# Kernel optimization log

Measured on AMD Instinct MI355X. Metric: run time of the kernel, lower is better.

Reference implementation:

```python
import jax, jax.numpy as jnp
import numpy as np

N_NODES = 50000
N_EDGES = 600000
D = 128
REL_DIM = 100
N_REL = 40
NEG_SLOPE = 0.2


def setup_inputs() -> dict:
    key = jax.random.key(0)
    ks = jax.random.split(key, 9)
    return {
        "node_features": jax.random.normal(ks[0], (N_NODES, D), jnp.float32),
        "edge_index": jax.random.randint(ks[1], (2, N_EDGES), 0, N_NODES, jnp.int64 if jax.config.jax_enable_x64 else jnp.int32),
        "edge_type": jax.random.randint(ks[2], (N_EDGES,), 0, N_REL, jnp.int32),
        "W": jax.random.normal(ks[3], (D, D), jnp.float32) * (1.0 / np.sqrt(D)),
        "W_r": jax.random.normal(ks[4], (REL_DIM, D), jnp.float32) * (1.0 / np.sqrt(REL_DIM)),
        "a": jax.random.normal(ks[5], (3 * D,), jnp.float32) * (1.0 / np.sqrt(3 * D)),
        "W_res": jax.random.normal(ks[6], (D, D), jnp.float32) * (1.0 / np.sqrt(D)),
        "b_res": jax.random.normal(ks[7], (D,), jnp.float32) * 0.01,
        "rel_emb": jax.random.normal(ks[8], (N_REL, REL_DIM), jnp.float32),
    }


def _segment_softmax(logits, seg_ids, num_segments):
    # numerically stable softmax over edges grouped by destination node
    seg_max = jax.ops.segment_max(logits, seg_ids, num_segments=num_segments)
    seg_max = jnp.where(jnp.isfinite(seg_max), seg_max, 0.0)
    e = jnp.exp(logits - seg_max[seg_ids])
    seg_sum = jax.ops.segment_sum(e, seg_ids, num_segments=num_segments)
    return e / (seg_sum[seg_ids] + 1e-16)


def reference(node_features, edge_index, edge_type, W, W_r, a, W_res, b_res, rel_emb):
    src = edge_index[0]  # x_j (source / message sender)
    dst = edge_index[1]  # x_i (target / aggregation index)

    h = node_features @ W                      # [N, D]
    h_rel = rel_emb[edge_type] @ W_r           # [E, D]
    h_src = h[src]                             # [E, D]
    h_dst = h[dst]                             # [E, D]

    # attention logit per edge: a . cat(W x_i, W x_j, W_r r_e), LeakyReLU(0.2)
    logit = h_dst @ a[:D] + h_src @ a[D:2 * D] + h_rel @ a[2 * D:]  # [E]
    logit = jax.nn.leaky_relu(logit, NEG_SLOPE)

    alpha = _segment_softmax(logit, dst, N_NODES)  # [E]

    agg = jax.ops.segment_sum(h_src * alpha[:, None], dst, num_segments=N_NODES)  # [N, D]

    out = agg + node_features @ W_res + b_res  # residual connection
    # LayerG: SELU then dropout (identity in eval mode)
    return jax.nn.selu(out)
```

## Files before the change

kernel.cpp:

```cpp
#include <hip/hip_runtime.h>
#include <hip/hip_bf16.h>

typedef __attribute__((ext_vector_type(8))) short bf16x8;
typedef __attribute__((ext_vector_type(4))) float f32x4;

#define LDS_STRIDE 528
#define CAP 64

__device__ __forceinline__ unsigned short f2bf(float f) {
    union { float f; unsigned int u; } v; v.f = f;
    unsigned int r = (v.u + 0x7FFF + ((v.u >> 16) & 1)) >> 16;
    return (unsigned short)r;
}
__device__ __forceinline__ float bf2f(unsigned int hbits) {
    union { unsigned int u; float f; } v; v.u = hbits << 16;
    return v.f;
}

__global__ __launch_bounds__(256) void setup_kernel(
    int* __restrict__ counts, int N,
    const float* __restrict__ W, const float* __restrict__ W_res,
    unsigned short* __restrict__ WbPack,
    const float* __restrict__ W_r, const float* __restrict__ a,
    const float* __restrict__ rel_emb, float* __restrict__ rl,
    int n_rel, int rel_dim, int zb)
{
    __shared__ float a3[128];
    __shared__ float wa[128];
    int bid = blockIdx.x;
    int tid = threadIdx.x;
    if (bid < zb) {
        int i = bid * 256 + tid;
        if (i < N) counts[i] = 0;
        return;
    }
    if (bid < zb + 16) {
        int g = (bid - zb) * 256 + tid;
        int t = g >> 8;
        int s = (g >> 6) & 3;
        int lane = g & 63;
        int ncol = ((t & 7) << 4) + (lane & 15);
        int k0 = s * 32 + ((lane >> 4) << 3);
        const float* srcw = (t < 8) ? W : W_res;
        unsigned short* dst = WbPack + ((size_t)(t * 4 + s) * 64 + lane) * 8;
        #pragma unroll
        for (int j = 0; j < 8; ++j) dst[j] = f2bf(srcw[(size_t)(k0 + j) * 128 + ncol]);
        return;
    }
    if (tid < 128) {
        a3[tid] = a[256 + tid];
    }
    __syncthreads();
    if (tid < rel_dim) {
        float s = 0.f;
        for (int d = 0; d < 128; ++d) s += W_r[tid * 128 + d] * a3[d];
        wa[tid] = s;
    }
    __syncthreads();
    if (tid < n_rel) {
        float s = 0.f;
        for (int k = 0; k < rel_dim; ++k) s += rel_emb[tid * rel_dim + k] * wa[k];
        rl[tid] = s;
    }
}

__global__ __launch_bounds__(256) void gemm_edge_kernel(
    const float* __restrict__ X, const unsigned short* __restrict__ WbPack,
    const float* __restrict__ b_res, const float* __restrict__ a,
    unsigned short* __restrict__ hb, unsigned short* __restrict__ resb,
    float* __restrict__ p, float* __restrict__ q, int M,
    const int* __restrict__ src, const int* __restrict__ dst_i, const int* __restrict__ etype,
    int* __restrict__ counts, unsigned int* __restrict__ slots, int E, int EB)
{
    __shared__ __align__(16) unsigned char smem[64 * LDS_STRIDE];
    __shared__ float pq_s[128];
    const int tid = threadIdx.x;
    const int bid = blockIdx.x;

    const bool is_edge = (bid < 2 * EB) && (bid & 1);
    if (is_edge) {
        const int base = (bid >> 1) * 2048 + tid;
        #pragma unroll
        for (int k = 0; k < 8; ++k) {
            int e = base + k * 256;
            if (e < E) {
                int d = __builtin_nontemporal_load(dst_i + e);
                int s = __builtin_nontemporal_load(src + e);
                int t = __builtin_nontemporal_load(etype + e);
                int rk = atomicAdd(&counts[d], 1);
                if (rk < CAP)
                    slots[(size_t)d * CAP + rk] = (unsigned int)s | ((unsigned int)t << 16);
            }
        }
        return;
    }
    const int gid = (bid < 2 * EB) ? (bid >> 1) : (bid - EB);

    const int lane = tid & 63;
    const int wave = tid >> 6;
    const int rowbase = gid * 64;
    const int c16 = lane & 15;
    const int kq = lane >> 4;

    if (tid < 128) pq_s[tid] = 0.f;

    bf16x8 wfrag[4][4];
    #pragma unroll
    for (int tt = 0; tt < 4; ++tt)
        #pragma unroll
        for (int s = 0; s < 4; ++s)
            wfrag[tt][s] = *(const bf16x8*)(WbPack + ((size_t)((wave * 4 + tt) * 4 + s) * 64 + lane) * 8);

    float bres[4];
    #pragma unroll
    for (int tt = 0; tt < 4; ++tt) {
        int t = wave * 4 + tt;
        bres[tt] = (t >= 8) ? b_res[(t - 8) * 16 + c16] : 0.f;
    }
    float pa[4], qa[4];
    #pragma unroll
    for (int tt = 0; tt < 4; ++tt) {
        int col = (wave * 4 + tt) * 16 + c16;
        pa[tt] = (wave < 2) ? a[col] : 0.f;
        qa[tt] = (wave < 2) ? a[128 + col] : 0.f;
    }

    #pragma unroll
    for (int j = 0; j < 8; ++j) {
        int ch = j * 256 + tid;
        int r = ch >> 5;
        int c = ch & 31;
        int gr = rowbase + r; if (gr >= M) gr = M - 1;
        float4 v = *(const float4*)(X + (size_t)gr * 128 + c * 4);
        unsigned int u0 = ((unsigned)f2bf(v.y) << 16) | f2bf(v.x);
        unsigned int u1 = ((unsigned)f2bf(v.w) << 16) | f2bf(v.z);
        *(uint2*)(smem + r * LDS_STRIDE + c * 8) = make_uint2(u0, u1);
    }
    __syncthreads();

    f32x4 acc[4][4];
    #pragma unroll
    for (int rt = 0; rt < 4; ++rt)
        #pragma unroll
        for (int tt = 0; tt < 4; ++tt) acc[rt][tt] = (f32x4){0.f, 0.f, 0.f, 0.f};

    #pragma unroll
    for (int s = 0; s < 4; ++s) {
        #pragma unroll
        for (int rt = 0; rt < 4; ++rt) {
            int row = rt * 16 + c16;
            bf16x8 af = *(const bf16x8*)(smem + row * LDS_STRIDE + s * 64 + kq * 16);
            #pragma unroll
            for (int tt = 0; tt < 4; ++tt)
                acc[rt][tt] = __builtin_amdgcn_mfma_f32_16x16x32_bf16(af, wfrag[tt][s], acc[rt][tt], 0, 0, 0);
        }
    }
    __syncthreads();

    if (wave < 2) {
        #pragma unroll
        for (int rt = 0; rt < 4; ++rt) {
            #pragma unroll
            for (int i = 0; i < 4; ++i) {
                float pp = 0.f, qq = 0.f;
                #pragma unroll
                for (int tt = 0; tt < 4; ++tt) {
                    pp += acc[rt][tt][i] * pa[tt];
                    qq += acc[rt][tt][i] * qa[tt];
                }
                #pragma unroll
                for (int d = 1; d < 16; d <<= 1) {
                    pp += __shfl_xor(pp, d, 64);
                    qq += __shfl_xor(qq, d, 64);
                }
                if (c16 == 0) {
                    int r = rt * 16 + kq * 4 + i;
                    atomicAdd(&pq_s[r], pp);
                    atomicAdd(&pq_s[64 + r], qq);
                }
            }
        }
    }

    #pragma unroll
    for (int rt = 0; rt < 4; ++rt) {
        #pragma unroll
        for (int tt = 0; tt < 4; ++tt) {
            int colall = (wave * 4 + tt) * 16 + c16;
            #pragma unroll
            for (int i = 0; i < 4; ++i) {
                int row = rt * 16 + kq * 4 + i;
                *(unsigned short*)(smem + row * LDS_STRIDE + colall * 2) = f2bf(acc[rt][tt][i] + bres[tt]);
            }
        }
    }
    __syncthreads();

    #pragma unroll
    for (int j = 0; j < 4; ++j) {
        int ch = j * 256 + tid;
        int r = ch >> 4;
        int c = ch & 15;
        int gr = rowbase + r;
        uint4 hv = *(const uint4*)(smem + r * LDS_STRIDE + c * 16);
        uint4 rv = *(const uint4*)(smem + r * LDS_STRIDE + 256 + c * 16);
        if (gr < M) {
            *(uint4*)(hb + (size_t)gr * 128 + c * 8) = hv;
            *(uint4*)(resb + (size_t)gr * 128 + c * 8) = rv;
        }
    }
    if (tid < 64) {
        int gr = rowbase + tid;
        if (gr < M) { p[gr] = pq_s[tid]; q[gr] = pq_s[64 + tid]; }
    }
}

__global__ __launch_bounds__(256) void agg_kernel(
    const unsigned short* __restrict__ hb, const unsigned short* __restrict__ resb,
    const float* __restrict__ p, const float* __restrict__ q, const float* __restrict__ rl,
    const int* __restrict__ counts, const unsigned int* __restrict__ slots,
    float* __restrict__ out, int N, int n_rel)
{
    __shared__ float rls[64];
    if (threadIdx.x < n_rel) rls[threadIdx.x] = rl[threadIdx.x];
    __syncthreads();

    const int tid = threadIdx.x;
    const int lane = tid & 63;
    const int sub = lane & 31;
    const int shbase = lane & 32;
    int node = blockIdx.x * 8 + ((tid >> 6) << 1) + (lane >> 5);
    if (node >= N) return;
    int nn = min(counts[node], CAP);

    float pnode = p[node];
    float a0 = 0.f, a1 = 0.f, a2 = 0.f, a3 = 0.f;
    float ssum = 0.f;
    const unsigned short* hsub = hb + sub * 4;

    for (int c = 0; c < nn; c += 32) {
        int m = min(32, nn - c);
        float se = 0.f;
        int sv = 0;
        if (sub < m) {
            unsigned int pk = slots[(size_t)node * CAP + c + sub];
            sv = (int)(pk & 0xffffu);
            int t = (int)(pk >> 16);
            float l = pnode + q[sv] + rls[t];
            l = (l > 0.f) ? l : 0.2f * l;
            se = __expf(l);
        }
        ssum += se;

        int j = 0;
        for (; j + 7 < m; j += 8) {
            float w[8]; int r[8]; uint2 v[8];
            #pragma unroll
            for (int u = 0; u < 8; ++u) { w[u] = __shfl(se, shbase + j + u); r[u] = __shfl(sv, shbase + j + u); }
            #pragma unroll
            for (int u = 0; u < 8; ++u) v[u] = *(const uint2*)(hsub + (size_t)r[u] * 128);
            #pragma unroll
            for (int u = 0; u < 8; ++u) {
                a0 += w[u] * bf2f(v[u].x & 0xffff);
                a1 += w[u] * bf2f(v[u].x >> 16);
                a2 += w[u] * bf2f(v[u].y & 0xffff);
                a3 += w[u] * bf2f(v[u].y >> 16);
            }
        }
        for (; j + 3 < m; j += 4) {
            float w[4]; int r[4]; uint2 v[4];
            #pragma unroll
            for (int u = 0; u < 4; ++u) { w[u] = __shfl(se, shbase + j + u); r[u] = __shfl(sv, shbase + j + u); }
            #pragma unroll
            for (int u = 0; u < 4; ++u) v[u] = *(const uint2*)(hsub + (size_t)r[u] * 128);
            #pragma unroll
            for (int u = 0; u < 4; ++u) {
                a0 += w[u] * bf2f(v[u].x & 0xffff);
                a1 += w[u] * bf2f(v[u].x >> 16);
                a2 += w[u] * bf2f(v[u].y & 0xffff);
                a3 += w[u] * bf2f(v[u].y >> 16);
            }
        }
        for (; j < m; ++j) {
            float w = __shfl(se, shbase + j);
            int r = __shfl(sv, shbase + j);
            uint2 v = *(const uint2*)(hsub + (size_t)r * 128);
            a0 += w * bf2f(v.x & 0xffff);
            a1 += w * bf2f(v.x >> 16);
            a2 += w * bf2f(v.y & 0xffff);
            a3 += w * bf2f(v.y >> 16);
        }
    }

    #pragma unroll
    for (int d = 1; d < 32; d <<= 1) ssum += __shfl_xor(ssum, d, 64);
    float inv = 1.0f / (ssum + 1e-16f);
    a0 *= inv; a1 *= inv; a2 *= inv; a3 *= inv;

    uint2 rv = *(const uint2*)(resb + (size_t)node * 128 + sub * 4);
    float o0 = a0 + bf2f(rv.x & 0xffff), o1 = a1 + bf2f(rv.x >> 16);
    float o2 = a2 + bf2f(rv.y & 0xffff), o3 = a3 + bf2f(rv.y >> 16);
    const float SC = 1.0507009873554805f, AL = 1.6732632423543772f;
    o0 = (o0 > 0.f) ? SC * o0 : SC * AL * (__expf(o0) - 1.f);
    o1 = (o1 > 0.f) ? SC * o1 : SC * AL * (__expf(o1) - 1.f);
    o2 = (o2 > 0.f) ? SC * o2 : SC * AL * (__expf(o2) - 1.f);
    o3 = (o3 > 0.f) ? SC * o3 : SC * AL * (__expf(o3) - 1.f);
    f32x4 ov = (f32x4){o0, o1, o2, o3};
    __builtin_nontemporal_store(ov, (f32x4*)(out + (size_t)node * 128 + sub * 4));
}

extern "C" void kernel_launch(void* const* d_in, const int* in_sizes, int n_in,
                              void* d_out, int out_size, void* d_ws, size_t ws_size,
                              hipStream_t stream)
{
    const float* X      = (const float*)d_in[0];
    const int*   ei     = (const int*)d_in[1];
    const int*   etype  = (const int*)d_in[2];
    const float* W      = (const float*)d_in[3];
    const float* W_r    = (const float*)d_in[4];
    const float* a      = (const float*)d_in[5];
    const float* W_res  = (const float*)d_in[6];
    const float* b_res  = (const float*)d_in[7];
    const float* rel_emb= (const float*)d_in[8];

    const int N = in_sizes[0] / 128;
    const int E = in_sizes[2];
    const int n_rel = in_sizes[8] / 100;
    const int* src = ei;
    const int* dst = ei + E;

    char* w = (char*)d_ws;
    auto alloc = [&](size_t bytes) -> void* {
        void* ptr = (void*)w;
        w += (bytes + 255) & ~(size_t)255;
        return ptr;
    };
    unsigned short* WbPack = (unsigned short*)alloc((size_t)16 * 4 * 64 * 8 * 2);
    unsigned short* hb     = (unsigned short*)alloc((size_t)N * 128 * 2);
    unsigned short* resb   = (unsigned short*)alloc((size_t)N * 128 * 2);
    float* p       = (float*)alloc((size_t)N * 4);
    float* q       = (float*)alloc((size_t)N * 4);
    float* rl      = (float*)alloc(64 * 4);
    int*   counts  = (int*)alloc((size_t)N * 4);
    unsigned int* slots = (unsigned int*)alloc((size_t)N * CAP * 4);
    float* out     = (float*)d_out;

    const int zb = (N + 255) / 256;
    const int gemm_blocks = (N + 63) / 64;
    const int agg_blocks = (N + 7) / 8;
    const int edge_blocks = (E + 2047) / 2048;
    const int fused_blocks = gemm_blocks + edge_blocks;

    setup_kernel<<<zb + 17, 256, 0, stream>>>(counts, N, W, W_res, WbPack,
                                              W_r, a, rel_emb, rl, n_rel, 100, zb);
    gemm_edge_kernel<<<fused_blocks, 256, 0, stream>>>(X, WbPack, b_res, a, hb, resb, p, q, N,
                                                       src, dst, etype, counts, slots, E, edge_blocks);
    agg_kernel<<<agg_blocks, 256, 0, stream>>>(hb, resb, p, q, rl, counts, slots, out, N, n_rel);
}
```

Baseline: 173.6 us.

## Fold edge bucketing into every GEMM block instead of separate edge blocks

Drops the interleaved edge-only blocks and gives each GEMM block a share of edges (up to 1024). The edge indices are loaded at kernel start into registers and scattered with atomics after the GEMM epilogue, so the load latency hides behind the matmul. This cuts the block count and the idle edge blocks, but adds register pressure (12 ints per thread). It also assumes EPB stays at or below 1024, which holds here (E/gemm_blocks rounds up to 768).

```diff
diff --git a/kernel.cpp b/kernel.cpp
--- a/kernel.cpp
+++ b/kernel.cpp
@@ -70,31 +70,24 @@
     unsigned short* __restrict__ hb, unsigned short* __restrict__ resb,
     float* __restrict__ p, float* __restrict__ q, int M,
     const int* __restrict__ src, const int* __restrict__ dst_i, const int* __restrict__ etype,
-    int* __restrict__ counts, unsigned int* __restrict__ slots, int E, int EB)
+    int* __restrict__ counts, unsigned int* __restrict__ slots, int E, int EPB)
 {
     __shared__ __align__(16) unsigned char smem[64 * LDS_STRIDE];
     __shared__ float pq_s[128];
     const int tid = threadIdx.x;
-    const int bid = blockIdx.x;
-
-    const bool is_edge = (bid < 2 * EB) && (bid & 1);
-    if (is_edge) {
-        const int base = (bid >> 1) * 2048 + tid;
-        #pragma unroll
-        for (int k = 0; k < 8; ++k) {
-            int e = base + k * 256;
-            if (e < E) {
-                int d = __builtin_nontemporal_load(dst_i + e);
-                int s = __builtin_nontemporal_load(src + e);
-                int t = __builtin_nontemporal_load(etype + e);
-                int rk = atomicAdd(&counts[d], 1);
-                if (rk < CAP)
-                    slots[(size_t)d * CAP + rk] = (unsigned int)s | ((unsigned int)t << 16);
-            }
-        }
-        return;
-    }
-    const int gid = (bid < 2 * EB) ? (bid >> 1) : (bid - EB);
+    const int gid = blockIdx.x;
+
+    int ed[4]; int es[4]; int et[4];
+    #pragma unroll
+    for (int k = 0; k < 4; ++k) {
+        ed[k] = -1; es[k] = 0; et[k] = 0;
+        int e = gid * EPB + k * 256 + tid;
+        if (k * 256 < EPB && e < E) {
+            ed[k] = __builtin_nontemporal_load(dst_i + e);
+            es[k] = __builtin_nontemporal_load(src + e);
+            et[k] = __builtin_nontemporal_load(etype + e);
+        }
+    }
 
     const int lane = tid & 63;
     const int wave = tid >> 6;
@@ -213,6 +206,16 @@
         int gr = rowbase + tid;
         if (gr < M) { p[gr] = pq_s[tid]; q[gr] = pq_s[64 + tid]; }
     }
+
+    #pragma unroll
+    for (int k = 0; k < 4; ++k) {
+        if (ed[k] >= 0) {
+            int rk = atomicAdd(&counts[ed[k]], 1);
+            if (rk < CAP)
+                slots[(size_t)ed[k] * CAP + rk] =
+                    (unsigned int)es[k] | ((unsigned int)et[k] << 16);
+        }
+    }
 }
 
 __global__ __launch_bounds__(256) void agg_kernel(
@@ -348,12 +351,11 @@
     const int zb = (N + 255) / 256;
     const int gemm_blocks = (N + 63) / 64;
     const int agg_blocks = (N + 7) / 8;
-    const int edge_blocks = (E + 2047) / 2048;
-    const int fused_blocks = gemm_blocks + edge_blocks;
+    const int EPB = (((E + gemm_blocks - 1) / gemm_blocks) + 255) & ~255;
 
     setup_kernel<<<zb + 17, 256, 0, stream>>>(counts, N, W, W_res, WbPack,
                                               W_r, a, rel_emb, rl, n_rel, 100, zb);
-    gemm_edge_kernel<<<fused_blocks, 256, 0, stream>>>(X, WbPack, b_res, a, hb, resb, p, q, N,
-                                                       src, dst, etype, counts, slots, E, edge_blocks);
+    gemm_edge_kernel<<<gemm_blocks, 256, 0, stream>>>(X, WbPack, b_res, a, hb, resb, p, q, N,
+                                                      src, dst, etype, counts, slots, E, EPB);
     agg_kernel<<<agg_blocks, 256, 0, stream>>>(hb, resb, p, q, rl, counts, slots, out, N, n_rel);
 }
```

After: 181.2 us. 4.4% more time.

## Replace global atomic edge bucketing with two-level radix binning via LDS atomics

Applied to the files above, without the earlier changes.

Swaps per-destination global atomicAdd slot insertion for a counting-sort pipeline. A histogram pass counts edges per 256-node bucket per chunk, a single-block prefix scan computes offsets, and a scatter pass writes packed edges into bucket order using LDS atomics. A place kernel then fills the per-node slots with LDS counters. The goal is to remove contended random global atomics and scattered writes. The cost is two extra kernel launches, an extra pass over dst, a serial single-block prefix scan, and the packing relies on src < 65536 and etype < 64.

```diff
diff --git a/kernel.cpp b/kernel.cpp
--- a/kernel.cpp
+++ b/kernel.cpp
@@ -6,6 +6,7 @@
 
 #define LDS_STRIDE 528
 #define CAP 64
+#define CHUNK 4096
 
 __device__ __forceinline__ unsigned short f2bf(float f) {
     union { float f; unsigned int u; } v; v.f = f;
@@ -18,83 +19,129 @@
 }
 
 __global__ __launch_bounds__(256) void setup_kernel(
-    int* __restrict__ counts, int N,
     const float* __restrict__ W, const float* __restrict__ W_res,
     unsigned short* __restrict__ WbPack,
     const float* __restrict__ W_r, const float* __restrict__ a,
     const float* __restrict__ rel_emb, float* __restrict__ rl,
-    int n_rel, int rel_dim, int zb)
+    int n_rel, int rel_dim,
+    const int* __restrict__ dst_i, unsigned int* __restrict__ cnt,
+    int E, int NBLK, int NBUCK)
 {
     __shared__ float a3[128];
     __shared__ float wa[128];
+    __shared__ unsigned int hist[256];
     int bid = blockIdx.x;
     int tid = threadIdx.x;
-    if (bid < zb) {
-        int i = bid * 256 + tid;
-        if (i < N) counts[i] = 0;
-        return;
-    }
-    if (bid < zb + 16) {
-        int g = (bid - zb) * 256 + tid;
+
+    if (bid < 16) {
+        int g = bid * 256 + tid;
         int t = g >> 8;
         int s = (g >> 6) & 3;
         int lane = g & 63;
         int ncol = ((t & 7) << 4) + (lane & 15);
         int k0 = s * 32 + ((lane >> 4) << 3);
         const float* srcw = (t < 8) ? W : W_res;
-        unsigned short* dst = WbPack + ((size_t)(t * 4 + s) * 64 + lane) * 8;
-        #pragma unroll
-        for (int j = 0; j < 8; ++j) dst[j] = f2bf(srcw[(size_t)(k0 + j) * 128 + ncol]);
+        unsigned short* dstp = WbPack + ((size_t)(t * 4 + s) * 64 + lane) * 8;
+        #pragma unroll
+        for (int j = 0; j < 8; ++j) dstp[j] = f2bf(srcw[(size_t)(k0 + j) * 128 + ncol]);
         return;
     }
-    if (tid < 128) {
-        a3[tid] = a[256 + tid];
-    }
-    __syncthreads();
-    if (tid < rel_dim) {
-        float s = 0.f;
-        for (int d = 0; d < 128; ++d) s += W_r[tid * 128 + d] * a3[d];
-        wa[tid] = s;
-    }
-    __syncthreads();
-    if (tid < n_rel) {
-        float s = 0.f;
-        for (int k = 0; k < rel_dim; ++k) s += rel_emb[tid * rel_dim + k] * wa[k];
-        rl[tid] = s;
-    }
-}
-
-__global__ __launch_bounds__(256) void gemm_edge_kernel(
+    if (bid == 16) {
+        if (tid < 128) a3[tid] = a[256 + tid];
+        __syncthreads();
+        if (tid < rel_dim) {
+            float s = 0.f;
+            for (int d = 0; d < 128; ++d) s += W_r[tid * 128 + d] * a3[d];
+            wa[tid] = s;
+        }
+        __syncthreads();
+        if (tid < n_rel) {
+            float s = 0.f;
+            for (int k = 0; k < rel_dim; ++k) s += rel_emb[tid * rel_dim + k] * wa[k];
+            rl[tid] = s;
+        }
+        return;
+    }
+    const int k = bid - 17;
+    hist[tid] = 0;
+    __syncthreads();
+    #pragma unroll
+    for (int i = 0; i < CHUNK / 256; ++i) {
+        int e = k * CHUNK + i * 256 + tid;
+        if (e < E) atomicAdd(&hist[((unsigned int)dst_i[e]) >> 8], 1u);
+    }
+    __syncthreads();
+    if (tid < NBUCK) cnt[(size_t)tid * NBLK + k] = hist[tid];
+}
+
+__global__ __launch_bounds__(256) void prefix_kernel(
+    const unsigned int* __restrict__ cnt, unsigned int* __restrict__ start,
+    unsigned int* __restrict__ base, unsigned int* __restrict__ total,
+    int NBLK, int NBUCK)
+{
+    __shared__ unsigned int tot_s[256];
+    const int b = threadIdx.x;
+    unsigned int run = 0;
+    if (b < NBUCK) {
+        #pragma unroll 4
+        for (int k = 0; k < NBLK; ++k) {
+            unsigned int v = cnt[(size_t)b * NBLK + k];
+            start[(size_t)b * NBLK + k] = run;
+            run += v;
+        }
+    }
+    tot_s[threadIdx.x] = run;
+    __syncthreads();
+    if (threadIdx.x == 0) {
+        unsigned int acc = 0;
+        for (int i = 0; i < NBUCK; ++i) { unsigned int t = tot_s[i]; tot_s[i] = acc; acc += t; }
+    }
+    __syncthreads();
+    if (b < NBUCK) {
+        unsigned int mybase = tot_s[b];
+        base[b] = mybase;
+        total[b] = run;
+        #pragma unroll 4
+        for (int k = 0; k < NBLK; ++k) start[(size_t)b * NBLK + k] += mybase;
+    }
+}
+
+__global__ __launch_bounds__(256) void gemm_scatter_kernel(
     const float* __restrict__ X, const unsigned short* __restrict__ WbPack,
     const float* __restrict__ b_res, const float* __restrict__ a,
     unsigned short* __restrict__ hb, unsigned short* __restrict__ resb,
     float* __restrict__ p, float* __restrict__ q, int M,
     const int* __restrict__ src, const int* __restrict__ dst_i, const int* __restrict__ etype,
-    int* __restrict__ counts, unsigned int* __restrict__ slots, int E, int EB)
+    const unsigned int* __restrict__ start, unsigned int* __restrict__ binned,
+    int E, int NC, int NBUCK)
 {
     __shared__ __align__(16) unsigned char smem[64 * LDS_STRIDE];
     __shared__ float pq_s[128];
     const int tid = threadIdx.x;
     const int bid = blockIdx.x;
 
-    const bool is_edge = (bid < 2 * EB) && (bid & 1);
-    if (is_edge) {
-        const int base = (bid >> 1) * 2048 + tid;
-        #pragma unroll
-        for (int k = 0; k < 8; ++k) {
-            int e = base + k * 256;
+    const bool isC = (bid < 2 * NC) && (bid & 1);
+    if (isC) {
+        const int k = bid >> 1;
+        unsigned int* lds = (unsigned int*)smem;
+        lds[tid] = 0;
+        if (tid < NBUCK) lds[256 + tid] = start[(size_t)tid * NC + k];
+        __syncthreads();
+        #pragma unroll
+        for (int i = 0; i < CHUNK / 256; ++i) {
+            int e = k * CHUNK + i * 256 + tid;
             if (e < E) {
-                int d = __builtin_nontemporal_load(dst_i + e);
-                int s = __builtin_nontemporal_load(src + e);
-                int t = __builtin_nontemporal_load(etype + e);
-                int rk = atomicAdd(&counts[d], 1);
-                if (rk < CAP)
-                    slots[(size_t)d * CAP + rk] = (unsigned int)s | ((unsigned int)t << 16);
+                unsigned int d = (unsigned int)dst_i[e];
+                unsigned int bk = d >> 8;
+                unsigned int s = (unsigned int)src[e];
+                unsigned int t = (unsigned int)etype[e];
+                unsigned int r = atomicAdd(&lds[bk], 1u);
+                binned[lds[256 + bk] + r] = (s << 16) | ((t & 63u) << 10) | (d & 255u);
             }
         }
         return;
     }
-    const int gid = (bid < 2 * EB) ? (bid >> 1) : (bid - EB);
+    const int gid = (bid < 2 * NC) ? (bid >> 1) : (bid - NC);
 
     const int lane = tid & 63;
     const int wave = tid >> 6;
@@ -215,6 +262,30 @@
     }
 }
 
+__global__ __launch_bounds__(256) void place_kernel(
+    const unsigned int* __restrict__ binned,
+    const unsigned int* __restrict__ base, const unsigned int* __restrict__ total,
+    unsigned int* __restrict__ slots, int* __restrict__ counts, int N)
+{
+    __shared__ unsigned int c256[256];
+    const int b = blockIdx.x;
+    const int tid = threadIdx.x;
+    c256[tid] = 0;
+    __syncthreads();
+    const unsigned int off = base[b];
+    const unsigned int nE = total[b];
+    for (unsigned int i = tid; i < nE; i += 256) {
+        unsigned int pk = binned[off + i];
+        unsigned int dl = pk & 255u;
+        unsigned int r = atomicAdd(&c256[dl], 1u);
+        if (r < CAP)
+            slots[((size_t)b * 256 + dl) * CAP + r] = (pk >> 16) | (((pk >> 10) & 63u) << 16);
+    }
+    __syncthreads();
+    int node = b * 256 + tid;
+    if (node < N) counts[node] = (int)c256[tid];
+}
+
 __global__ __launch_bounds__(256) void agg_kernel(
     const unsigned short* __restrict__ hb, const unsigned short* __restrict__ resb,
     const float* __restrict__ p, const float* __restrict__ q, const float* __restrict__ rl,
@@ -335,6 +406,9 @@
         w += (bytes + 255) & ~(size_t)255;
         return ptr;
     };
+    const int NBLK  = (E + CHUNK - 1) / CHUNK;
+    const int NBUCK = (N + 255) >> 8;
+
     unsigned short* WbPack = (unsigned short*)alloc((size_t)16 * 4 * 64 * 8 * 2);
     unsigned short* hb     = (unsigned short*)alloc((size_t)N * 128 * 2);
     unsigned short* resb   = (unsigned short*)alloc((size_t)N * 128 * 2);
@@ -342,18 +416,23 @@
     float* q       = (float*)alloc((size_t)N * 4);
     float* rl      = (float*)alloc(64 * 4);
     int*   counts  = (int*)alloc((size_t)N * 4);
-    unsigned int* slots = (unsigned int*)alloc((size_t)N * CAP * 4);
+    unsigned int* slots  = (unsigned int*)alloc((size_t)N * CAP * 4);
+    unsigned int* cnt    = (unsigned int*)alloc((size_t)NBUCK * NBLK * 4);
+    unsigned int* startg = (unsigned int*)alloc((size_t)NBUCK * NBLK * 4);
+    unsigned int* baseg  = (unsigned int*)alloc((size_t)NBUCK * 4);
+    unsigned int* totalg = (unsigned int*)alloc((size_t)NBUCK * 4);
+    unsigned int* binned = (unsigned int*)alloc((size_t)E * 4);
     float* out     = (float*)d_out;
 
-    const int zb = (N + 255) / 256;
     const int gemm_blocks = (N + 63) / 64;
-    const int agg_blocks = (N + 7) / 8;
-    const int edge_blocks = (E + 2047) / 2048;
-    const int fused_blocks = gemm_blocks + edge_blocks;
-
-    setup_kernel<<<zb + 17, 256, 0, stream>>>(counts, N, W, W_res, WbPack,
-                                              W_r, a, rel_emb, rl, n_rel, 100, zb);
-    gemm_edge_kernel<<<fused_blocks, 256, 0, stream>>>(X, WbPack, b_res, a, hb, resb, p, q, N,
-                                                       src, dst, etype, counts, slots, E, edge_blocks);
+    const int agg_blocks  = (N + 7) / 8;
+
+    setup_kernel<<<17 + NBLK, 256, 0, stream>>>(W, W_res, WbPack, W_r, a, rel_emb, rl,
+                                                n_rel, 100, dst, cnt, E, NBLK, NBUCK);
+    prefix_kernel<<<1, 256, 0, stream>>>(cnt, startg, baseg, totalg, NBLK, NBUCK);
+    gemm_scatter_kernel<<<gemm_blocks + NBLK, 256, 0, stream>>>(
+        X, WbPack, b_res, a, hb, resb, p, q, N,
+        src, dst, etype, startg, binned, E, NBLK, NBUCK);
+    place_kernel<<<NBUCK, 256, 0, stream>>>(binned, baseg, totalg, slots, counts, N);
     agg_kernel<<<agg_blocks, 256, 0, stream>>>(hb, resb, p, q, rl, counts, slots, out, N, n_rel);
 }
```

Measured after the change: 191.2 us. 1.1x slower.
